# Performance work log

Hardware: AMD Instinct MI355X
Metric: run time of the kernel (lower is better)

## Reference

```python
import jax, jax.numpy as jnp
import numpy as np

D_MODEL = 2048
D_FF = 8192
BATCH = 4
SEQ = 2048
MAX_EXP = 4
NUM_BITS = 8
C_CHUNKS = 2
SCALE = 0.1


def _pow2_ternary(key, out_dim, in_dim, max_exp):
    """Weights are t * 2^{-e}: ternary sign times power-of-two magnitude."""
    k1, k2 = jax.random.split(key)
    t = jax.random.randint(k1, (out_dim, in_dim), -1, 2).astype(jnp.float32)
    e = jax.random.randint(k2, (out_dim, in_dim), 0, max_exp + 1).astype(jnp.float32)
    return t * jnp.exp2(-e)


def setup_inputs() -> dict:
    key = jax.random.key(0)
    kx, k1, k2 = jax.random.split(key, 3)
    x = jax.random.normal(kx, (BATCH, SEQ, D_MODEL), dtype=jnp.float32)
    W1 = _pow2_ternary(k1, D_FF, D_MODEL, MAX_EXP)   # [d_ff, d_model] torch-style
    W2 = _pow2_ternary(k2, D_MODEL, D_FF, MAX_EXP)   # [d_model, d_ff]
    return {"x": x, "W1": W1, "W2": W2}


def _lookup_act(h):
    # 16-bit (num_bits * c) fixed-point quantize, then table-valued GELU.
    total_bits = NUM_BITS * C_CHUNKS
    qmax = 2 ** (total_bits - 1) - 1
    qmin = -(2 ** (total_bits - 1))
    q = jnp.clip(jnp.round(h / SCALE), qmin, qmax)
    return jax.nn.gelu(q * SCALE)


def reference(x, W1, W2):
    # fc1: [b,s,d_model] x [d_ff,d_model]^T -> [b,s,d_ff]
    h = jnp.einsum('bsd,fd->bsf', x, W1)
    a = _lookup_act(h)
    # fc2: [b,s,d_ff] x [d_model,d_ff]^T -> [b,s,d_model]
    return jnp.einsum('bsf,df->bsd', a, W2)
```

## Files before the change

kernel.cpp:

```cpp
#include <hip/hip_runtime.h>
#include <cstdint>
#include <cstddef>


typedef __bf16 bf16_t;
typedef bf16_t bf16x8 __attribute__((ext_vector_type(8)));
typedef float  floatx4 __attribute__((ext_vector_type(4)));

#define AS1 __attribute__((address_space(1)))
#define AS3 __attribute__((address_space(3)))

__device__ __forceinline__ void async_cp16(const void* g, void* l) {
    __builtin_amdgcn_global_load_lds((const AS1 void*)g, (AS3 void*)l, 16, 0, 0);
}

__device__ __forceinline__ float gelu_fast(float x) {
    const float C0 = 1.5957691216057308f;
    const float C1 = 0.0713548163f;
    float u2 = x * fmaf(C1, x * x, C0);
    float e  = __expf(u2);
    float r  = __builtin_amdgcn_rcpf(1.0f + e);
    return x * (1.0f - r);
}

__global__ __launch_bounds__(256)
void cvt_pack_swz(const float* __restrict__ src, bf16_t* __restrict__ dst,
                  int K, int tshift)
{
    const size_t   oc = (size_t)blockIdx.x * 256 + threadIdx.x;
    const uint32_t ho = ((uint32_t)oc & 1023u) * 16u;
    const size_t   region = oc >> 10;
    const int      h  = (int)(region & 1);
    const size_t   pt = region >> 1;
    const int      t  = (int)(pt & ((1u << tshift) - 1));
    const size_t   p  = pt >> tshift;
    const uint32_t L = ho ^ (((ho >> 9) & 1u) << 5);
    const int      s = (int)(L >> 10);
    const uint32_t u = L & 1023u;
    const size_t   row = p * 256 + (size_t)(h * 128 + (s >> 1) * 16 + (int)(u >> 6));
    const int      k   = (t << 6) + (s & 1) * 32 + (int)((u & 63u) >> 1);
    const float* sp = src + row * (size_t)K + k;
    float4 a = *(const float4*)sp;
    float4 b = *(const float4*)(sp + 4);
    bf16x8 o;
    o[0] = (bf16_t)a.x; o[1] = (bf16_t)a.y; o[2] = (bf16_t)a.z; o[3] = (bf16_t)a.w;
    o[4] = (bf16_t)b.x; o[5] = (bf16_t)b.y; o[6] = (bf16_t)b.z; o[7] = (bf16_t)b.w;
    *(bf16x8*)(dst + oc * 8) = o;
}

template<bool ACT, typename OutT>
__global__ __launch_bounds__(512, 2)
void gemm256(const bf16_t* __restrict__ A, const bf16_t* __restrict__ B,
             OutT* __restrict__ C, int M, int N, int K, int nbxs)
{
    __shared__ __align__(16) bf16_t lds[65536];
    char* const ldsb = (char*)lds;

    const int NT  = K >> 6;
    const int id  = blockIdx.x;
    const int nwg = gridDim.x;
    const int sw = (id & 7) * (nwg >> 3) + (id >> 3);
    const int by = sw >> nbxs;
    const int bx = sw & ((1 << nbxs) - 1);

    const int tid  = threadIdx.x;
    const int lane = tid & 63;
    const int wave = tid >> 6;
    const int wm = wave >> 2;
    const int wn = wave & 3;

    const bf16_t* const Ap = A + (size_t)by * NT * 16384;
    const bf16_t* const Bp = B + (size_t)bx * NT * 16384;

    uint32_t lsw = (uint32_t)(((lane & 15) << 6) + ((lane >> 4) << 4));
    lsw ^= ((lsw >> 9) & 1u) << 5;

    const uint32_t aBase = (uint32_t)(2 + wm) << 14;
    const uint32_t bBase = (uint32_t)(wn >> 1) << 14;
    const int bSub = (wn & 1) * 4;

    floatx4 acc[8][4];
    #pragma unroll
    for (int i = 0; i < 8; ++i)
      #pragma unroll
      for (int j = 0; j < 4; ++j)
        acc[i][j] = (floatx4)0.0f;

    auto stage = [&](int t, int j) {
        const bf16_t* g = (j < 2) ? (Bp + (size_t)t * 16384 + (size_t)j * 8192)
                                  : (Ap + (size_t)t * 16384 + (size_t)(j - 2) * 8192);
        char* l = ldsb + (((t & 1) << 16) + (j << 14));
        async_cp16((const char*)g + tid * 16, l + tid * 16);
        async_cp16((const char*)g + 8192 + tid * 16, l + 8192 + tid * 16);
    };

    stage(0, 0); stage(0, 1); stage(0, 2); stage(0, 3);
    stage(1, 0); stage(1, 1); stage(1, 2);
    asm volatile("s_waitcnt vmcnt(6)" ::: "memory");
    __builtin_amdgcn_s_barrier();

    for (int t = 0; t < NT; ++t) {
        const char* aB = ldsb + ((t & 1) << 16) + aBase;
        const char* bB = ldsb + ((t & 1) << 16) + bBase;
        const bool s1 = (t + 1 < NT);
        const bool s2 = (t + 2 < NT);

        bf16x8 af[4][2], bfr[4][2];

        #pragma unroll
        for (int fm = 0; fm < 4; ++fm)
          #pragma unroll
          for (int ks = 0; ks < 2; ++ks)
            af[fm][ks] = *(const bf16x8*)(aB + ((((fm << 1) + ks) << 10) | lsw));
        #pragma unroll
        for (int fn = 0; fn < 4; ++fn)
          #pragma unroll
          for (int ks = 0; ks < 2; ++ks)
            bfr[fn][ks] = *(const bf16x8*)(bB + (((((bSub + fn) << 1) + ks) << 10) | lsw));
        if (s1) stage(t + 1, 3);
        __builtin_amdgcn_s_barrier();
        __builtin_amdgcn_s_setprio(1);
        #pragma unroll
        for (int ks = 0; ks < 2; ++ks)
          #pragma unroll
          for (int fm = 0; fm < 4; ++fm)
            #pragma unroll
            for (int fn = 0; fn < 2; ++fn)
              acc[fm][fn] = __builtin_amdgcn_mfma_f32_16x16x32_bf16(
                  af[fm][ks], bfr[fn][ks], acc[fm][fn], 0, 0, 0);
        __builtin_amdgcn_s_setprio(0);
        asm volatile("s_waitcnt lgkmcnt(0)" ::: "memory");
        __builtin_amdgcn_s_barrier();

        if (s2) stage(t + 2, 0);
        __builtin_amdgcn_s_barrier();
        __builtin_amdgcn_s_setprio(1);
        #pragma unroll
        for (int ks = 0; ks < 2; ++ks)
          #pragma unroll
          for (int fm = 0; fm < 4; ++fm)
            #pragma unroll
            for (int fn = 2; fn < 4; ++fn)
              acc[fm][fn] = __builtin_amdgcn_mfma_f32_16x16x32_bf16(
                  af[fm][ks], bfr[fn][ks], acc[fm][fn], 0, 0, 0);
        __builtin_amdgcn_s_setprio(0);
        __builtin_amdgcn_s_barrier();

        #pragma unroll
        for (int fm = 0; fm < 4; ++fm)
          #pragma unroll
          for (int ks = 0; ks < 2; ++ks)
            af[fm][ks] = *(const bf16x8*)(aB + (((((4 + fm) << 1) + ks) << 10) | lsw));
        if (s2) stage(t + 2, 1);
        __builtin_amdgcn_s_barrier();
        __builtin_amdgcn_s_setprio(1);
        #pragma unroll
        for (int ks = 0; ks < 2; ++ks)
          #pragma unroll
          for (int fm = 0; fm < 4; ++fm)
            #pragma unroll
            for (int fn = 0; fn < 2; ++fn)
              acc[4 + fm][fn] = __builtin_amdgcn_mfma_f32_16x16x32_bf16(
                  af[fm][ks], bfr[fn][ks], acc[4 + fm][fn], 0, 0, 0);
        __builtin_amdgcn_s_setprio(0);
        __builtin_amdgcn_s_barrier();

        if (s2) stage(t + 2, 2);
        __builtin_amdgcn_s_barrier();
        __builtin_amdgcn_s_setprio(1);
        #pragma unroll
        for (int ks = 0; ks < 2; ++ks)
          #pragma unroll
          for (int fm = 0; fm < 4; ++fm)
            #pragma unroll
            for (int fn = 2; fn < 4; ++fn)
              acc[4 + fm][fn] = __builtin_amdgcn_mfma_f32_16x16x32_bf16(
                  af[fm][ks], bfr[fn][ks], acc[4 + fm][fn], 0, 0, 0);
        __builtin_amdgcn_s_setprio(0);
        if (s2)      asm volatile("s_waitcnt vmcnt(6)" ::: "memory");
        else if (s1) asm volatile("s_waitcnt vmcnt(0)" ::: "memory");
        __builtin_amdgcn_s_barrier();
    }

    if constexpr (ACT) {
        __syncthreads();
        const uint32_t rbase = (uint32_t)(wn * 2 + wm) << 14;
        #pragma unroll
        for (int fm = 0; fm < 8; ++fm)
          #pragma unroll
          for (int fn = 0; fn < 4; ++fn)
            #pragma unroll
            for (int r = 0; r < 4; ++r) {
                float h = acc[fm][fn][r];
                float q = rintf(h * 10.0f);
                q = fminf(fmaxf(q, -32768.0f), 32767.0f);
                h = gelu_fast(q * 0.1f);
                uint32_t L = ((uint32_t)((fm << 1) + (fn >> 1)) << 10)
                           + (uint32_t)((((lane >> 4) << 2) + r) << 6)
                           + (uint32_t)((((fn & 1) << 4) + (lane & 15)) << 1);
                uint32_t P = L ^ (((L >> 9) & 1u) << 5);
                *(bf16_t*)(ldsb + rbase + P) = (bf16_t)h;
            }
        __syncthreads();
        const int nkt2 = N >> 6;
        bf16_t* const Cb = (bf16_t*)C;
        #pragma unroll
        for (int it = 0; it < 16; ++it) {
            const int ch = it * 512 + tid;
            const int rg = ch >> 10;
            const int c  = ch & 1023;
            const size_t gr = ((size_t)by * nkt2 + (size_t)(bx * 4) + (rg >> 1)) * 2
                            + (size_t)(rg & 1);
            bf16x8 v = *(const bf16x8*)(ldsb + (size_t)ch * 16);
            *(bf16x8*)((char*)Cb + gr * 16384 + (size_t)c * 16) = v;
        }
    } else {
        const int r0 = by * 256 + wm * 128;
        const int c0 = bx * 256 + wn * 64;
        #pragma unroll
        for (int fm = 0; fm < 8; ++fm)
          #pragma unroll
          for (int fn = 0; fn < 4; ++fn) {
            const int col = c0 + fn * 16 + (lane & 15);
            #pragma unroll
            for (int r = 0; r < 4; ++r) {
              const int row = r0 + fm * 16 + ((lane >> 4) << 2) + r;
              C[(size_t)row * N + col] = (OutT)acc[fm][fn][r];
            }
          }
    }
}

extern "C" void kernel_launch(void* const* d_in, const int* in_sizes, int n_in,
                              void* d_out, int out_size, void* d_ws, size_t ws_size,
                              hipStream_t stream)
{
    const int M  = 8192;
    const int DM = 2048;
    const int DF = 8192;

    const float* x  = (const float*)d_in[0];
    const float* W1 = (const float*)d_in[1];
    const float* W2 = (const float*)d_in[2];
    float* out = (float*)d_out;

    bf16_t* xb  = (bf16_t*)d_ws;
    bf16_t* w1b = xb  + (size_t)M  * DM;
    bf16_t* w2b = w1b + (size_t)DF * DM;
    bf16_t* act = w2b + (size_t)DM * DF;

    cvt_pack_swz<<<8192, 256, 0, stream>>>(x,  xb,  DM, 5);
    cvt_pack_swz<<<8192, 256, 0, stream>>>(W1, w1b, DM, 5);
    cvt_pack_swz<<<8192, 256, 0, stream>>>(W2, w2b, DF, 7);

    gemm256<true, bf16_t><<<dim3(1024), 512, 0, stream>>>(xb, w1b, act, M, DF, DM, 5);
    gemm256<false, float><<<dim3(256), 512, 0, stream>>>(act, w2b, out, M, DM, DF, 3);
}
```

Before: 677.7 us.

## Restructure GEMM main loop to cut barriers and prefetch next B fragments

Result: faster. 638.0 us (-5.9%).

```diff
diff --git a/kernel.cpp b/kernel.cpp
--- a/kernel.cpp
+++ b/kernel.cpp
@@ -95,30 +95,37 @@
     };
 
     stage(0, 0); stage(0, 1); stage(0, 2); stage(0, 3);
-    stage(1, 0); stage(1, 1); stage(1, 2);
-    asm volatile("s_waitcnt vmcnt(6)" ::: "memory");
+    stage(1, 0); stage(1, 1); stage(1, 2); stage(1, 3);
+    asm volatile("s_waitcnt vmcnt(8)" ::: "memory");
     __builtin_amdgcn_s_barrier();
 
+    bf16x8 b01[2][2];
+    {
+        const char* bB0 = ldsb + bBase;
+        #pragma unroll
+        for (int fn = 0; fn < 2; ++fn)
+          #pragma unroll
+          for (int ks = 0; ks < 2; ++ks)
+            b01[fn][ks] = *(const bf16x8*)(bB0 + (((((bSub + fn) << 1) + ks) << 10) | lsw));
+    }
+
     for (int t = 0; t < NT; ++t) {
-        const char* aB = ldsb + ((t & 1) << 16) + aBase;
-        const char* bB = ldsb + ((t & 1) << 16) + bBase;
+        const char* aB  = ldsb + ((t & 1) << 16) + aBase;
+        const char* bBc = ldsb + ((t & 1) << 16) + bBase;
         const bool s1 = (t + 1 < NT);
         const bool s2 = (t + 2 < NT);
 
-        bf16x8 af[4][2], bfr[4][2];
-
+        bf16x8 af[4][2], b23[2][2];
         #pragma unroll
         for (int fm = 0; fm < 4; ++fm)
           #pragma unroll
           for (int ks = 0; ks < 2; ++ks)
             af[fm][ks] = *(const bf16x8*)(aB + ((((fm << 1) + ks) << 10) | lsw));
         #pragma unroll
-        for (int fn = 0; fn < 4; ++fn)
-          #pragma unroll
-          for (int ks = 0; ks < 2; ++ks)
-            bfr[fn][ks] = *(const bf16x8*)(bB + (((((bSub + fn) << 1) + ks) << 10) | lsw));
-        if (s1) stage(t + 1, 3);
-        __builtin_amdgcn_s_barrier();
+        for (int fn = 0; fn < 2; ++fn)
+          #pragma unroll
+          for (int ks = 0; ks < 2; ++ks)
+            b23[fn][ks] = *(const bf16x8*)(bBc + (((((bSub + 2 + fn) << 1) + ks) << 10) | lsw));
         __builtin_amdgcn_s_setprio(1);
         #pragma unroll
         for (int ks = 0; ks < 2; ++ks)
@@ -127,32 +134,29 @@
             #pragma unroll
             for (int fn = 0; fn < 2; ++fn)
               acc[fm][fn] = __builtin_amdgcn_mfma_f32_16x16x32_bf16(
-                  af[fm][ks], bfr[fn][ks], acc[fm][fn], 0, 0, 0);
-        __builtin_amdgcn_s_setprio(0);
+                  af[fm][ks], b01[fn][ks], acc[fm][fn], 0, 0, 0);
+        __builtin_amdgcn_s_setprio(0);
+
         asm volatile("s_waitcnt lgkmcnt(0)" ::: "memory");
         __builtin_amdgcn_s_barrier();
-
-        if (s2) stage(t + 2, 0);
-        __builtin_amdgcn_s_barrier();
-        __builtin_amdgcn_s_setprio(1);
-        #pragma unroll
-        for (int ks = 0; ks < 2; ++ks)
-          #pragma unroll
-          for (int fm = 0; fm < 4; ++fm)
-            #pragma unroll
-            for (int fn = 2; fn < 4; ++fn)
-              acc[fm][fn] = __builtin_amdgcn_mfma_f32_16x16x32_bf16(
-                  af[fm][ks], bfr[fn][ks], acc[fm][fn], 0, 0, 0);
-        __builtin_amdgcn_s_setprio(0);
-        __builtin_amdgcn_s_barrier();
-
+        if (s2) { stage(t + 2, 0); stage(t + 2, 1); }
+        __builtin_amdgcn_s_setprio(1);
+        #pragma unroll
+        for (int ks = 0; ks < 2; ++ks)
+          #pragma unroll
+          for (int fm = 0; fm < 4; ++fm)
+            #pragma unroll
+            for (int fn = 0; fn < 2; ++fn)
+              acc[fm][2 + fn] = __builtin_amdgcn_mfma_f32_16x16x32_bf16(
+                  af[fm][ks], b23[fn][ks], acc[fm][2 + fn], 0, 0, 0);
+        __builtin_amdgcn_s_setprio(0);
+
+        bf16x8 ah[4][2];
         #pragma unroll
         for (int fm = 0; fm < 4; ++fm)
           #pragma unroll
           for (int ks = 0; ks < 2; ++ks)
-            af[fm][ks] = *(const bf16x8*)(aB + (((((4 + fm) << 1) + ks) << 10) | lsw));
-        if (s2) stage(t + 2, 1);
-        __builtin_amdgcn_s_barrier();
+            ah[fm][ks] = *(const bf16x8*)(aB + (((((4 + fm) << 1) + ks) << 10) | lsw));
         __builtin_amdgcn_s_setprio(1);
         #pragma unroll
         for (int ks = 0; ks < 2; ++ks)
@@ -161,25 +165,31 @@
             #pragma unroll
             for (int fn = 0; fn < 2; ++fn)
               acc[4 + fm][fn] = __builtin_amdgcn_mfma_f32_16x16x32_bf16(
-                  af[fm][ks], bfr[fn][ks], acc[4 + fm][fn], 0, 0, 0);
-        __builtin_amdgcn_s_setprio(0);
-        __builtin_amdgcn_s_barrier();
-
-        if (s2) stage(t + 2, 2);
-        __builtin_amdgcn_s_barrier();
-        __builtin_amdgcn_s_setprio(1);
-        #pragma unroll
-        for (int ks = 0; ks < 2; ++ks)
-          #pragma unroll
-          for (int fm = 0; fm < 4; ++fm)
-            #pragma unroll
-            for (int fn = 2; fn < 4; ++fn)
-              acc[4 + fm][fn] = __builtin_amdgcn_mfma_f32_16x16x32_bf16(
-                  af[fm][ks], bfr[fn][ks], acc[4 + fm][fn], 0, 0, 0);
-        __builtin_amdgcn_s_setprio(0);
-        if (s2)      asm volatile("s_waitcnt vmcnt(6)" ::: "memory");
+                  ah[fm][ks], b01[fn][ks], acc[4 + fm][fn], 0, 0, 0);
+        __builtin_amdgcn_s_setprio(0);
+
+        if (s2)      asm volatile("s_waitcnt vmcnt(4)" ::: "memory");
         else if (s1) asm volatile("s_waitcnt vmcnt(0)" ::: "memory");
         __builtin_amdgcn_s_barrier();
+        if (s1) {
+            const char* bBn = ldsb + (((t + 1) & 1) << 16) + bBase;
+            #pragma unroll
+            for (int fn = 0; fn < 2; ++fn)
+              #pragma unroll
+              for (int ks = 0; ks < 2; ++ks)
+                b01[fn][ks] = *(const bf16x8*)(bBn + (((((bSub + fn) << 1) + ks) << 10) | lsw));
+        }
+        if (s2) { stage(t + 2, 2); stage(t + 2, 3); }
+        __builtin_amdgcn_s_setprio(1);
+        #pragma unroll
+        for (int ks = 0; ks < 2; ++ks)
+          #pragma unroll
+          for (int fm = 0; fm < 4; ++fm)
+            #pragma unroll
+            for (int fn = 0; fn < 2; ++fn)
+              acc[4 + fm][2 + fn] = __builtin_amdgcn_mfma_f32_16x16x32_bf16(
+                  ah[fm][ks], b23[fn][ks], acc[4 + fm][2 + fn], 0, 0, 0);
+        __builtin_amdgcn_s_setprio(0);
     }
 
     if constexpr (ACT) {
```

## Shrink GEMM tiles to 128x128 with simpler double buffering and XCD-aware grouping

Applied to the files above, without the earlier changes.

After: 699.1 us. +3.2%, slower.

```diff
diff --git a/kernel.cpp b/kernel.cpp
--- a/kernel.cpp
+++ b/kernel.cpp
@@ -49,144 +49,98 @@
 }
 
 template<bool ACT, typename OutT>
-__global__ __launch_bounds__(512, 2)
-void gemm256(const bf16_t* __restrict__ A, const bf16_t* __restrict__ B,
-             OutT* __restrict__ C, int M, int N, int K, int nbxs)
+__global__ __launch_bounds__(512, 4)
+void gemm128(const bf16_t* __restrict__ A, const bf16_t* __restrict__ B,
+             OutT* __restrict__ C, int M, int N, int K,
+             int nsqpx, int sqxshift)
 {
-    __shared__ __align__(16) bf16_t lds[65536];
+    __shared__ __align__(16) bf16_t lds[32768];
     char* const ldsb = (char*)lds;
 
-    const int NT  = K >> 6;
-    const int id  = blockIdx.x;
-    const int nwg = gridDim.x;
-    const int sw = (id & 7) * (nwg >> 3) + (id >> 3);
-    const int by = sw >> nbxs;
-    const int bx = sw & ((1 << nbxs) - 1);
+    const int NT = K >> 6;
+
+    const int j   = blockIdx.x;
+    const int xcd = j & 7;
+    const int loc = j >> 3;
+    const int sq  = loc >> 6;
+    const int jj  = loc & 63;
+    const int sqg = xcd * nsqpx + sq;
+    const int sqy = sqg >> sqxshift;
+    const int sqx = sqg & ((1 << sqxshift) - 1);
+    const int by  = sqy * 8 + (jj >> 3);
+    const int bx  = sqx * 8 + (jj & 7);
 
     const int tid  = threadIdx.x;
     const int lane = tid & 63;
     const int wave = tid >> 6;
-    const int wm = wave >> 2;
-    const int wn = wave & 3;
-
-    const bf16_t* const Ap = A + (size_t)by * NT * 16384;
-    const bf16_t* const Bp = B + (size_t)bx * NT * 16384;
+    const int wm = wave >> 1;
+    const int wn = wave & 1;
+
+    const bf16_t* const Ap = A + (size_t)(by >> 1) * NT * 16384
+                               + (size_t)(by & 1) * 8192;
+    const bf16_t* const Bp = B + (size_t)(bx >> 1) * NT * 16384
+                               + (size_t)(bx & 1) * 8192;
 
     uint32_t lsw = (uint32_t)(((lane & 15) << 6) + ((lane >> 4) << 4));
     lsw ^= ((lsw >> 9) & 1u) << 5;
 
-    const uint32_t aBase = (uint32_t)(2 + wm) << 14;
-    const uint32_t bBase = (uint32_t)(wn >> 1) << 14;
-    const int bSub = (wn & 1) * 4;
-
-    floatx4 acc[8][4];
+    floatx4 acc[2][4];
     #pragma unroll
-    for (int i = 0; i < 8; ++i)
+    for (int i = 0; i < 2; ++i)
       #pragma unroll
-      for (int j = 0; j < 4; ++j)
-        acc[i][j] = (floatx4)0.0f;
-
-    auto stage = [&](int t, int j) {
-        const bf16_t* g = (j < 2) ? (Bp + (size_t)t * 16384 + (size_t)j * 8192)
-                                  : (Ap + (size_t)t * 16384 + (size_t)(j - 2) * 8192);
-        char* l = ldsb + (((t & 1) << 16) + (j << 14));
-        async_cp16((const char*)g + tid * 16, l + tid * 16);
-        async_cp16((const char*)g + 8192 + tid * 16, l + 8192 + tid * 16);
+      for (int jn = 0; jn < 4; ++jn)
+        acc[i][jn] = (floatx4)0.0f;
+
+    auto stage = [&](int t) {
+        const char* ga = (const char*)(Ap + (size_t)t * 16384);
+        const char* gb = (const char*)(Bp + (size_t)t * 16384);
+        char* base = ldsb + ((t & 1) << 15);
+        async_cp16(ga + tid * 16, base + tid * 16);
+        async_cp16(ga + 8192 + tid * 16, base + 8192 + tid * 16);
+        async_cp16(gb + tid * 16, base + 16384 + tid * 16);
+        async_cp16(gb + 8192 + tid * 16, base + 16384 + 8192 + tid * 16);
     };
 
-    stage(0, 0); stage(0, 1); stage(0, 2); stage(0, 3);
-    stage(1, 0); stage(1, 1); stage(1, 2);
-    asm volatile("s_waitcnt vmcnt(6)" ::: "memory");
+    stage(0);
+    asm volatile("s_waitcnt vmcnt(0)" ::: "memory");
     __builtin_amdgcn_s_barrier();
 
     for (int t = 0; t < NT; ++t) {
-        const char* aB = ldsb + ((t & 1) << 16) + aBase;
-        const char* bB = ldsb + ((t & 1) << 16) + bBase;
         const bool s1 = (t + 1 < NT);
-        const bool s2 = (t + 2 < NT);
-
-        bf16x8 af[4][2], bfr[4][2];
-
-        #pragma unroll
-        for (int fm = 0; fm < 4; ++fm)
+        if (s1) stage(t + 1);
+
+        const char* aB = ldsb + ((t & 1) << 15);
+        const char* bB = aB + 16384;
+        bf16x8 af[2][2], bf[4][2];
+        #pragma unroll
+        for (int fm = 0; fm < 2; ++fm)
           #pragma unroll
           for (int ks = 0; ks < 2; ++ks)
-            af[fm][ks] = *(const bf16x8*)(aB + ((((fm << 1) + ks) << 10) | lsw));
+            af[fm][ks] = *(const bf16x8*)(aB + (((((wm << 1) + fm) << 1) + ks) << 10 | lsw));
         #pragma unroll
         for (int fn = 0; fn < 4; ++fn)
           #pragma unroll
           for (int ks = 0; ks < 2; ++ks)
-            bfr[fn][ks] = *(const bf16x8*)(bB + (((((bSub + fn) << 1) + ks) << 10) | lsw));
-        if (s1) stage(t + 1, 3);
-        __builtin_amdgcn_s_barrier();
+            bf[fn][ks] = *(const bf16x8*)(bB + (((((wn << 2) + fn) << 1) + ks) << 10 | lsw));
+
         __builtin_amdgcn_s_setprio(1);
         #pragma unroll
         for (int ks = 0; ks < 2; ++ks)
           #pragma unroll
-          for (int fm = 0; fm < 4; ++fm)
+          for (int fm = 0; fm < 2; ++fm)
             #pragma unroll
-            for (int fn = 0; fn < 2; ++fn)
+            for (int fn = 0; fn < 4; ++fn)
               acc[fm][fn] = __builtin_amdgcn_mfma_f32_16x16x32_bf16(
-                  af[fm][ks], bfr[fn][ks], acc[fm][fn], 0, 0, 0);
+                  af[fm][ks], bf[fn][ks], acc[fm][fn], 0, 0, 0);
         __builtin_amdgcn_s_setprio(0);
-        asm volatile("s_waitcnt lgkmcnt(0)" ::: "memory");
-        __builtin_amdgcn_s_barrier();
-
-        if (s2) stage(t + 2, 0);
-        __builtin_amdgcn_s_barrier();
-        __builtin_amdgcn_s_setprio(1);
-        #pragma unroll
-        for (int ks = 0; ks < 2; ++ks)
-          #pragma unroll
-          for (int fm = 0; fm < 4; ++fm)
-            #pragma unroll
-            for (int fn = 2; fn < 4; ++fn)
-              acc[fm][fn] = __builtin_amdgcn_mfma_f32_16x16x32_bf16(
-                  af[fm][ks], bfr[fn][ks], acc[fm][fn], 0, 0, 0);
-        __builtin_amdgcn_s_setprio(0);
-        __builtin_amdgcn_s_barrier();
-
-        #pragma unroll
-        for (int fm = 0; fm < 4; ++fm)
-          #pragma unroll
-          for (int ks = 0; ks < 2; ++ks)
-            af[fm][ks] = *(const bf16x8*)(aB + (((((4 + fm) << 1) + ks) << 10) | lsw));
-        if (s2) stage(t + 2, 1);
-        __builtin_amdgcn_s_barrier();
-        __builtin_amdgcn_s_setprio(1);
-        #pragma unroll
-        for (int ks = 0; ks < 2; ++ks)
-          #pragma unroll
-          for (int fm = 0; fm < 4; ++fm)
-            #pragma unroll
-            for (int fn = 0; fn < 2; ++fn)
-              acc[4 + fm][fn] = __builtin_amdgcn_mfma_f32_16x16x32_bf16(
-                  af[fm][ks], bfr[fn][ks], acc[4 + fm][fn], 0, 0, 0);
-        __builtin_amdgcn_s_setprio(0);
-        __builtin_amdgcn_s_barrier();
-
-        if (s2) stage(t + 2, 2);
-        __builtin_amdgcn_s_barrier();
-        __builtin_amdgcn_s_setprio(1);
-        #pragma unroll
-        for (int ks = 0; ks < 2; ++ks)
-          #pragma unroll
-          for (int fm = 0; fm < 4; ++fm)
-            #pragma unroll
-            for (int fn = 2; fn < 4; ++fn)
-              acc[4 + fm][fn] = __builtin_amdgcn_mfma_f32_16x16x32_bf16(
-                  af[fm][ks], bfr[fn][ks], acc[4 + fm][fn], 0, 0, 0);
-        __builtin_amdgcn_s_setprio(0);
-        if (s2)      asm volatile("s_waitcnt vmcnt(6)" ::: "memory");
-        else if (s1) asm volatile("s_waitcnt vmcnt(0)" ::: "memory");
+
+        if (s1) asm volatile("s_waitcnt vmcnt(0)" ::: "memory");
         __builtin_amdgcn_s_barrier();
     }
 
     if constexpr (ACT) {
-        __syncthreads();
-        const uint32_t rbase = (uint32_t)(wn * 2 + wm) << 14;
-        #pragma unroll
-        for (int fm = 0; fm < 8; ++fm)
+        #pragma unroll
+        for (int fm = 0; fm < 2; ++fm)
           #pragma unroll
           for (int fn = 0; fn < 4; ++fn)
             #pragma unroll
@@ -195,30 +149,28 @@
                 float q = rintf(h * 10.0f);
                 q = fminf(fmaxf(q, -32768.0f), 32767.0f);
                 h = gelu_fast(q * 0.1f);
-                uint32_t L = ((uint32_t)((fm << 1) + (fn >> 1)) << 10)
+                uint32_t L = ((uint32_t)((((wm << 1) + fm) << 1) + (fn >> 1)) << 10)
                            + (uint32_t)((((lane >> 4) << 2) + r) << 6)
                            + (uint32_t)((((fn & 1) << 4) + (lane & 15)) << 1);
                 uint32_t P = L ^ (((L >> 9) & 1u) << 5);
-                *(bf16_t*)(ldsb + rbase + P) = (bf16_t)h;
+                *(bf16_t*)(ldsb + ((uint32_t)wn << 14) + P) = (bf16_t)h;
             }
         __syncthreads();
         const int nkt2 = N >> 6;
-        bf16_t* const Cb = (bf16_t*)C;
-        #pragma unroll
-        for (int it = 0; it < 16; ++it) {
-            const int ch = it * 512 + tid;
-            const int rg = ch >> 10;
-            const int c  = ch & 1023;
-            const size_t gr = ((size_t)by * nkt2 + (size_t)(bx * 4) + (rg >> 1)) * 2
-                            + (size_t)(rg & 1);
-            bf16x8 v = *(const bf16x8*)(ldsb + (size_t)ch * 16);
-            *(bf16x8*)((char*)Cb + gr * 16384 + (size_t)c * 16) = v;
+        #pragma unroll
+        for (int it = 0; it < 4; ++it) {
+            const int ch  = it * 512 + tid;
+            const int tau = ch >> 10;
+            const int c   = ch & 1023;
+            const size_t gbyte = ((size_t)(by >> 1) * nkt2 + (size_t)(bx * 2 + tau)) * 32768
+                               + (size_t)(by & 1) * 16384 + (size_t)c * 16;
+            *(bf16x8*)((char*)C + gbyte) = *(const bf16x8*)(ldsb + (size_t)ch * 16);
         }
     } else {
-        const int r0 = by * 256 + wm * 128;
-        const int c0 = bx * 256 + wn * 64;
-        #pragma unroll
-        for (int fm = 0; fm < 8; ++fm)
+        const int r0 = by * 128 + wm * 32;
+        const int c0 = bx * 128 + wn * 64;
+        #pragma unroll
+        for (int fm = 0; fm < 2; ++fm)
           #pragma unroll
           for (int fn = 0; fn < 4; ++fn) {
             const int col = c0 + fn * 16 + (lane & 15);
@@ -253,6 +205,8 @@
     cvt_pack_swz<<<8192, 256, 0, stream>>>(W1, w1b, DM, 5);
     cvt_pack_swz<<<8192, 256, 0, stream>>>(W2, w2b, DF, 7);
 
-    gemm256<true, bf16_t><<<dim3(1024), 512, 0, stream>>>(xb, w1b, act, M, DF, DM, 5);
-    gemm256<false, float><<<dim3(256), 512, 0, stream>>>(act, w2b, out, M, DM, DF, 3);
-}
+    gemm128<true, bf16_t><<<dim3(4096), 512, 0, stream>>>(
+        xb, w1b, act, M, DF, DM, 8, 3);
+    gemm128<false, float><<<dim3(1024), 512, 0, stream>>>(
+        act, w2b, out, M, DM, DF, 2, 1);
+}
```
